# Performance work log

Measured on AMD Instinct MI355X. Metric: run time of the kernel, lower is better.

## Reference

```python
import jax, jax.numpy as jnp
import numpy as np

SPATIAL_SHAPES = [(128, 128), (64, 64), (32, 32), (16, 16)]  # (H_l, W_l) per level
NUM_HEADS = 8
NUM_LEVELS = 4
NUM_POINTS = 4
EMBED_DIM = 256
HEAD_DIM = EMBED_DIM // NUM_HEADS
LEN_V = sum(h * w for h, w in SPATIAL_SHAPES)  # 21760
BS, LQ = 8, 900


def setup_inputs() -> dict:
    key = jax.random.key(0)
    ks = jax.random.split(key, 12)
    s = 0.05
    return {
        'query': jax.random.normal(ks[0], (BS, LQ, EMBED_DIM), jnp.float32),
        'reference_points': jax.random.uniform(ks[1], (BS, LQ, NUM_LEVELS, 2), jnp.float32),
        'value': jax.random.normal(ks[2], (BS, LEN_V, EMBED_DIM), jnp.float32),
        'w_value': jax.random.normal(ks[3], (EMBED_DIM, EMBED_DIM), jnp.float32) * s,
        'b_value': jnp.zeros((EMBED_DIM,), jnp.float32),
        'w_off': jax.random.normal(ks[4], (EMBED_DIM, NUM_HEADS * NUM_LEVELS * NUM_POINTS * 2), jnp.float32) * s,
        'b_off': jax.random.normal(ks[5], (NUM_HEADS * NUM_LEVELS * NUM_POINTS * 2,), jnp.float32),
        'w_attn': jax.random.normal(ks[6], (EMBED_DIM, NUM_HEADS * NUM_LEVELS * NUM_POINTS), jnp.float32) * s,
        'b_attn': jnp.zeros((NUM_HEADS * NUM_LEVELS * NUM_POINTS,), jnp.float32),
        'w_out': jax.random.normal(ks[7], (EMBED_DIM, EMBED_DIM), jnp.float32) * s,
        'b_out': jnp.zeros((EMBED_DIM,), jnp.float32),
    }


def _bilinear_sample(val, locx, locy, H, W):
    # val: [bs, nh, H*W, hd]; locx/locy: [bs, nh, N] normalized in [0,1]
    # grid_sample semantics: align_corners=False, zero padding.
    px = locx * W - 0.5
    py = locy * H - 0.5
    x0 = jnp.floor(px)
    y0 = jnp.floor(py)
    dx = px - x0
    dy = py - y0
    x0i = x0.astype(jnp.int32)
    y0i = y0.astype(jnp.int32)
    out = jnp.zeros(val.shape[:2] + (locx.shape[-1], val.shape[-1]), val.dtype)
    corners = [
        (x0i, y0i, (1 - dx) * (1 - dy)),
        (x0i + 1, y0i, dx * (1 - dy)),
        (x0i, y0i + 1, (1 - dx) * dy),
        (x0i + 1, y0i + 1, dx * dy),
    ]
    for xi, yi, w in corners:
        valid = ((xi >= 0) & (xi < W) & (yi >= 0) & (yi < H)).astype(val.dtype)
        idx = jnp.clip(yi, 0, H - 1) * W + jnp.clip(xi, 0, W - 1)
        g = jnp.take_along_axis(val, idx[..., None], axis=2)  # [bs,nh,N,hd]
        out = out + g * (w * valid)[..., None]
    return out


def reference(query, reference_points, value, w_value, b_value, w_off, b_off,
              w_attn, b_attn, w_out, b_out):
    bs, Lq, C = query.shape
    # value projection -> [bs, Lv, nh, hd]
    v = (value @ w_value + b_value).reshape(bs, -1, NUM_HEADS, HEAD_DIM)
    # sampling offsets [bs,Lq,nh,L,P,2], attention weights softmax over L*P
    off = (query @ w_off + b_off).reshape(bs, Lq, NUM_HEADS, NUM_LEVELS, NUM_POINTS, 2)
    aw = (query @ w_attn + b_attn).reshape(bs, Lq, NUM_HEADS, NUM_LEVELS * NUM_POINTS)
    aw = jax.nn.softmax(aw, axis=-1).reshape(bs, Lq, NUM_HEADS, NUM_LEVELS, NUM_POINTS)
    # normalizer is (W_l, H_l) per level (flip of spatial shapes)
    norm = jnp.asarray([[w, h] for h, w in SPATIAL_SHAPES], query.dtype)  # [L,2]
    loc = reference_points[:, :, None, :, None, :] + off / norm[None, None, None, :, None, :]
    # per-level bilinear sampling and weighted reduction
    out = jnp.zeros((bs, Lq, NUM_HEADS, HEAD_DIM), query.dtype)
    start = 0
    for l, (H, W) in enumerate(SPATIAL_SHAPES):
        vl = v[:, start:start + H * W]                       # [bs,HW,nh,hd]
        vl = vl.transpose(0, 2, 1, 3)                        # [bs,nh,HW,hd]
        ll = loc[:, :, :, l].transpose(0, 2, 1, 3, 4)        # [bs,nh,Lq,P,2]
        ll = ll.reshape(bs, NUM_HEADS, Lq * NUM_POINTS, 2)
        s = _bilinear_sample(vl, ll[..., 0], ll[..., 1], H, W)
        s = s.reshape(bs, NUM_HEADS, Lq, NUM_POINTS, HEAD_DIM)
        out = out + jnp.einsum('bhqpd,bqhp->bqhd', s, aw[:, :, :, l])
        start += H * W
    out = out.reshape(bs, Lq, C)
    return out @ w_out + b_out
```

## Files before the change

kernel.cpp:

```cpp
#include <hip/hip_runtime.h>

#define BS 8
#define LQ 900
#define NH 8
#define NL 4
#define NP 4
#define HD 32
#define ED 256
#define LEN_V 21760

typedef __attribute__((ext_vector_type(8))) short bf16x8;
typedef __attribute__((ext_vector_type(4))) float f32x4;
typedef __attribute__((ext_vector_type(4))) float fv4;

static __device__ __forceinline__ unsigned short f2bf(float f) {
  union { float f; unsigned u; } x; x.f = f;
  unsigned r = x.u + 0x7fffu + ((x.u >> 16) & 1u);
  return (unsigned short)(r >> 16);
}
static __device__ __forceinline__ float bf2f(unsigned short s) {
  union { unsigned u; float f; } x; x.u = ((unsigned)s) << 16;
  return x.f;
}
static __device__ __forceinline__ unsigned pack2(float a, float b) {
  return (unsigned)f2bf(a) | ((unsigned)f2bf(b) << 16);
}
static __device__ __forceinline__ bf16x8 pack8(fv4 a, fv4 b) {
  union { uint4 u; bf16x8 h; } x;
  x.u.x = pack2(a.x, a.y);
  x.u.y = pack2(a.z, a.w);
  x.u.z = pack2(b.x, b.y);
  x.u.w = pack2(b.z, b.w);
  return x.h;
}

__global__ __launch_bounds__(256) void bprep_kernel(
    const float* __restrict__ w, unsigned short* __restrict__ Bsw) {
  const int id = blockIdx.x * 256 + threadIdx.x;
  const int n = id & 255;
  const int kseg = (id >> 8) & 3;
  const int kc = id >> 10;
  const float* src = &w[(kc * 32 + kseg * 8) * 256 + n];
  float f[8];
#pragma unroll
  for (int j = 0; j < 8; j++) f[j] = src[j * 256];
  uint4 pk;
  pk.x = pack2(f[0], f[1]);
  pk.y = pack2(f[2], f[3]);
  pk.z = pack2(f[4], f[5]);
  pk.w = pack2(f[6], f[7]);
  *(uint4*)&Bsw[((kc * 4 + kseg) * 256 + n) * 8] = pk;
}

__global__ __launch_bounds__(256, 3) void vproj_kernel(
    const float* __restrict__ value, const unsigned short* __restrict__ Bsw,
    const float* __restrict__ bias, unsigned short* __restrict__ vout) {
  const int t = threadIdx.x;
  const int row0 = blockIdx.x * 64;
  const int wv = t >> 6;
  const int lane = t & 63;
  const int quad = lane >> 4;
  const int nn = lane & 15;

  f32x4 acc[4][4];
#pragma unroll
  for (int i = 0; i < 4; i++)
#pragma unroll
    for (int j = 0; j < 4; j++) acc[i][j] = (f32x4)(0.f);

  const float* aptr = &value[(row0 + nn) * 256 + quad * 8];
  const unsigned short* bptr = &Bsw[(quad * 256 + wv * 64 + nn) * 8];

#pragma unroll
  for (int kc = 0; kc < 8; kc++) {
    bf16x8 af[4], bfr[4];
#pragma unroll
    for (int rt = 0; rt < 4; rt++) {
      const float* pa = aptr + rt * 16 * 256 + kc * 32;
      fv4 v0 = *(const fv4*)pa;
      fv4 v1 = *(const fv4*)(pa + 4);
      af[rt] = pack8(v0, v1);
    }
#pragma unroll
    for (int ct = 0; ct < 4; ct++)
      bfr[ct] = *(const bf16x8*)(bptr + (kc * 1024 + ct * 16) * 8);
#pragma unroll
    for (int rt = 0; rt < 4; rt++)
#pragma unroll
      for (int ct = 0; ct < 4; ct++)
        acc[rt][ct] = __builtin_amdgcn_mfma_f32_16x16x32_bf16(
            af[rt], bfr[ct], acc[rt][ct], 0, 0, 0);
  }

#pragma unroll
  for (int ct = 0; ct < 4; ct++) {
    const int col = wv * 64 + ct * 16 + nn;
    const float bv = bias[col];
    const int h = col >> 5;
    const int d = col & 31;
#pragma unroll
    for (int rt = 0; rt < 4; rt++) {
      f32x4 f = acc[rt][ct];
#pragma unroll
      for (int reg = 0; reg < 4; reg++) {
        const int grow = row0 + rt * 16 + quad * 4 + reg;
        const int b = grow / LEN_V;
        const int s = grow - b * LEN_V;
        vout[((b * NH + h) * LEN_V + s) * HD + d] = f2bf(f[reg] + bv);
      }
    }
  }
}

__global__ __launch_bounds__(384, 2) void offattn_kernel(
    const float* __restrict__ query,
    const float* __restrict__ w_off, const float* __restrict__ b_off,
    const float* __restrict__ w_attn, const float* __restrict__ b_attn,
    float* __restrict__ OFF, float* __restrict__ LOG) {
  const int t = threadIdx.x;
  const int row0 = blockIdx.x * 32;
  const int rg = t / 96;
  const int c4 = t % 96;
  const int col = c4 * 4;
  const bool isOff = col < 256;
  const float* wbase = isOff ? (w_off + col) : (w_attn + (col - 256));
  const int wstride = isOff ? 256 : 128;
  const float* bb = isOff ? (b_off + col) : (b_attn + (col - 256));
  __shared__ float a_lds[32][8];

  float4 acc[8];
#pragma unroll
  for (int r = 0; r < 8; r++) acc[r] = make_float4(0.f, 0.f, 0.f, 0.f);

  for (int k0 = 0; k0 < 256; k0 += 8) {
    __syncthreads();
    if (t < 256) a_lds[t >> 3][t & 7] = query[(row0 + (t >> 3)) * 256 + k0 + (t & 7)];
    __syncthreads();
    float4 wr[8];
#pragma unroll
    for (int k = 0; k < 8; k++)
      wr[k] = *(const float4*)&wbase[(k0 + k) * wstride];
#pragma unroll
    for (int r = 0; r < 8; r++) {
      const float* ar = &a_lds[rg * 8 + r][0];
      float4 a0 = *(const float4*)&ar[0];
      float4 a1 = *(const float4*)&ar[4];
      float4 s = acc[r];
      s.x += a0.x*wr[0].x + a0.y*wr[1].x + a0.z*wr[2].x + a0.w*wr[3].x
           + a1.x*wr[4].x + a1.y*wr[5].x + a1.z*wr[6].x + a1.w*wr[7].x;
      s.y += a0.x*wr[0].y + a0.y*wr[1].y + a0.z*wr[2].y + a0.w*wr[3].y
           + a1.x*wr[4].y + a1.y*wr[5].y + a1.z*wr[6].y + a1.w*wr[7].y;
      s.z += a0.x*wr[0].z + a0.y*wr[1].z + a0.z*wr[2].z + a0.w*wr[3].z
           + a1.x*wr[4].z + a1.y*wr[5].z + a1.z*wr[6].z + a1.w*wr[7].z;
      s.w += a0.x*wr[0].w + a0.y*wr[1].w + a0.z*wr[2].w + a0.w*wr[3].w
           + a1.x*wr[4].w + a1.y*wr[5].w + a1.z*wr[6].w + a1.w*wr[7].w;
      acc[r] = s;
    }
  }

  const float4 bv = *(const float4*)bb;
#pragma unroll
  for (int r = 0; r < 8; r++) {
    const int grow = row0 + rg * 8 + r;
    float4 o = make_float4(acc[r].x + bv.x, acc[r].y + bv.y,
                           acc[r].z + bv.z, acc[r].w + bv.w);
    if (isOff) *(float4*)&OFF[grow * 256 + col] = o;
    else       *(float4*)&LOG[grow * 128 + (col - 256)] = o;
  }
}

__global__ __launch_bounds__(256, 4) void sample_kernel(
    const float* __restrict__ refp, const unsigned short* __restrict__ vp,
    const float* __restrict__ OFF, const float* __restrict__ LOG,
    float* __restrict__ RES) {
  const int t = threadIdx.x;
  const int b = blockIdx.x / (LQ / 4);
  const int q0 = (blockIdx.x % (LQ / 4)) * 4;

  __shared__ float off_lds[4][256];
  __shared__ float aw_lds[4][128];
  __shared__ float ref_lds[4][4][2];
  __shared__ int   soff[512][4];
  __shared__ float swt[512][4];

#pragma unroll
  for (int qi = 0; qi < 4; qi++)
    off_lds[qi][t] = OFF[(b * LQ + q0 + qi) * 256 + t];
  if (t < 128) {
#pragma unroll
    for (int qi = 0; qi < 4; qi++)
      aw_lds[qi][t] = LOG[(b * LQ + q0 + qi) * 128 + t];
  }
  if (t < 32) {
    const int qi = t >> 3, l = (t >> 1) & 3, xy = t & 1;
    ref_lds[qi][l][xy] = refp[((b * LQ + q0 + qi) * NL + l) * 2 + xy];
  }
  __syncthreads();

  if (t < 32) {
    const int qi = t >> 3, h = t & 7;
    float* a = &aw_lds[qi][h * 16];
    float m = a[0];
#pragma unroll
    for (int i = 1; i < 16; i++) m = fmaxf(m, a[i]);
    float e[16];
    float ssum = 0.f;
#pragma unroll
    for (int i = 0; i < 16; i++) { e[i] = __expf(a[i] - m); ssum += e[i]; }
    const float inv = 1.f / ssum;
#pragma unroll
    for (int i = 0; i < 16; i++) a[i] = e[i] * inv;
  }
  __syncthreads();

#pragma unroll
  for (int ss = 0; ss < 2; ss++) {
    const int sid = t + ss * 256;
    const int p = sid & 3, l = (sid >> 2) & 3, h = (sid >> 4) & 7, qi = sid >> 7;
    const int W = 128 >> l;
    const int base = (l == 0) ? 0 : ((l == 1) ? 16384 : ((l == 2) ? 20480 : 21504));
    const float Wf = (float)W;
    const float refx = ref_lds[qi][l][0];
    const float refy = ref_lds[qi][l][1];
    const float offx = off_lds[qi][h * 32 + l * 8 + p * 2 + 0];
    const float offy = off_lds[qi][h * 32 + l * 8 + p * 2 + 1];
    const float aw = aw_lds[qi][h * 16 + l * 4 + p];
    const float px = refx * Wf + offx - 0.5f;
    const float py = refy * Wf + offy - 0.5f;
    const float x0f = floorf(px), y0f = floorf(py);
    const float dx = px - x0f, dy = py - y0f;
    const int x0 = (int)x0f, y0 = (int)y0f;
    const int x1 = x0 + 1, y1 = y0 + 1;
    const float mx0 = (x0 >= 0 && x0 < W) ? 1.f : 0.f;
    const float mx1 = (x1 >= 0 && x1 < W) ? 1.f : 0.f;
    const float my0 = (y0 >= 0 && y0 < W) ? 1.f : 0.f;
    const float my1 = (y1 >= 0 && y1 < W) ? 1.f : 0.f;
    const int x0c = min(max(x0, 0), W - 1);
    const int x1c = min(max(x1, 0), W - 1);
    const int y0c = min(max(y0, 0), W - 1);
    const int y1c = min(max(y1, 0), W - 1);
    soff[sid][0] = (base + y0c * W + x0c) * 16;
    soff[sid][1] = (base + y0c * W + x1c) * 16;
    soff[sid][2] = (base + y1c * W + x0c) * 16;
    soff[sid][3] = (base + y1c * W + x1c) * 16;
    swt[sid][0] = (1.f - dx) * (1.f - dy) * mx0 * my0 * aw;
    swt[sid][1] = dx * (1.f - dy) * mx1 * my0 * aw;
    swt[sid][2] = (1.f - dx) * dy * mx0 * my1 * aw;
    swt[sid][3] = dx * dy * mx1 * my1 * aw;
  }
  __syncthreads();

  const int qsel = t >> 7;
  const int hh = (t >> 4) & 7;
  const int d2 = t & 15;
  const unsigned* vpu = (const unsigned*)vp + (size_t)(b * NH + hh) * (LEN_V * HD / 2);
#pragma unroll
  for (int j = 0; j < 2; j++) {
    const int qi = qsel * 2 + j;
    float r0 = 0.f, r1 = 0.f;
#pragma unroll
    for (int lp = 0; lp < 16; lp++) {
      const int sid = ((qi * 8 + hh) << 4) + lp;
      const int4 o = *(const int4*)&soff[sid][0];
      const float4 w = *(const float4*)&swt[sid][0];
      const unsigned u00 = vpu[o.x + d2];
      const unsigned u10 = vpu[o.y + d2];
      const unsigned u01 = vpu[o.z + d2];
      const unsigned u11 = vpu[o.w + d2];
      r0 += w.x * bf2f((unsigned short)(u00 & 0xffff))
          + w.y * bf2f((unsigned short)(u10 & 0xffff))
          + w.z * bf2f((unsigned short)(u01 & 0xffff))
          + w.w * bf2f((unsigned short)(u11 & 0xffff));
      r1 += w.x * bf2f((unsigned short)(u00 >> 16))
          + w.y * bf2f((unsigned short)(u10 >> 16))
          + w.z * bf2f((unsigned short)(u01 >> 16))
          + w.w * bf2f((unsigned short)(u11 >> 16));
    }
    float2 rr = make_float2(r0, r1);
    *(float2*)&RES[(b * LQ + q0 + qi) * 256 + hh * 32 + d2 * 2] = rr;
  }
}

__global__ __launch_bounds__(256, 2) void outproj_kernel(
    const float* __restrict__ RES, const float* __restrict__ w,
    const float* __restrict__ bias, float* __restrict__ out) {
  const int t = threadIdx.x;
  const int row0 = blockIdx.x * 32;
  const int rg = t >> 6;
  const int c0 = (t & 63) << 2;
  __shared__ float a_lds[32][8];

  float4 acc[8];
#pragma unroll
  for (int r = 0; r < 8; r++) acc[r] = make_float4(0.f, 0.f, 0.f, 0.f);

  const int lr = t >> 3;
  const int lk = t & 7;
  for (int k0 = 0; k0 < 256; k0 += 8) {
    __syncthreads();
    a_lds[lr][lk] = RES[(row0 + lr) * 256 + k0 + lk];
    __syncthreads();
    float4 wr[8];
#pragma unroll
    for (int k = 0; k < 8; k++)
      wr[k] = *(const float4*)&w[(k0 + k) * 256 + c0];
#pragma unroll
    for (int r = 0; r < 8; r++) {
      const float* ar = &a_lds[rg * 8 + r][0];
      float4 a0 = *(const float4*)&ar[0];
      float4 a1 = *(const float4*)&ar[4];
      float4 s = acc[r];
      s.x += a0.x*wr[0].x + a0.y*wr[1].x + a0.z*wr[2].x + a0.w*wr[3].x
           + a1.x*wr[4].x + a1.y*wr[5].x + a1.z*wr[6].x + a1.w*wr[7].x;
      s.y += a0.x*wr[0].y + a0.y*wr[1].y + a0.z*wr[2].y + a0.w*wr[3].y
           + a1.x*wr[4].y + a1.y*wr[5].y + a1.z*wr[6].y + a1.w*wr[7].y;
      s.z += a0.x*wr[0].z + a0.y*wr[1].z + a0.z*wr[2].z + a0.w*wr[3].z
           + a1.x*wr[4].z + a1.y*wr[5].z + a1.z*wr[6].z + a1.w*wr[7].z;
      s.w += a0.x*wr[0].w + a0.y*wr[1].w + a0.z*wr[2].w + a0.w*wr[3].w
           + a1.x*wr[4].w + a1.y*wr[5].w + a1.z*wr[6].w + a1.w*wr[7].w;
      acc[r] = s;
    }
  }

  const float4 bv = *(const float4*)&bias[c0];
#pragma unroll
  for (int r = 0; r < 8; r++) {
    const int grow = row0 + rg * 8 + r;
    float4 o = make_float4(acc[r].x + bv.x, acc[r].y + bv.y,
                           acc[r].z + bv.z, acc[r].w + bv.w);
    *(float4*)&out[grow * 256 + c0] = o;
  }
}

extern "C" void kernel_launch(void* const* d_in, const int* in_sizes, int n_in,
                              void* d_out, int out_size, void* d_ws, size_t ws_size,
                              hipStream_t stream) {
  (void)in_sizes; (void)n_in; (void)out_size; (void)ws_size;
  const float* query   = (const float*)d_in[0];
  const float* refp    = (const float*)d_in[1];
  const float* value   = (const float*)d_in[2];
  const float* w_value = (const float*)d_in[3];
  const float* b_value = (const float*)d_in[4];
  const float* w_off   = (const float*)d_in[5];
  const float* b_off   = (const float*)d_in[6];
  const float* w_attn  = (const float*)d_in[7];
  const float* b_attn  = (const float*)d_in[8];
  const float* w_out   = (const float*)d_in[9];
  const float* b_out   = (const float*)d_in[10];
  float* out = (float*)d_out;

  char* ws = (char*)d_ws;
  unsigned short* vp = (unsigned short*)ws;
  float* OFF = (float*)(ws + 89128960);
  float* LOG = (float*)(ws + 89128960 + 7372800);
  float* RES = (float*)(ws + 89128960 + 7372800 + 3686400);
  unsigned short* Bsw = (unsigned short*)(ws + 89128960 + 7372800 + 3686400 + 7372800);

  bprep_kernel<<<32, 256, 0, stream>>>(w_value, Bsw);
  vproj_kernel<<<(BS * LEN_V) / 64, 256, 0, stream>>>(value, Bsw, b_value, vp);
  offattn_kernel<<<(BS * LQ) / 32, 384, 0, stream>>>(query, w_off, b_off,
                                                     w_attn, b_attn, OFF, LOG);
  sample_kernel<<<BS * (LQ / 4), 256, 0, stream>>>(refp, vp, OFF, LOG, RES);
  outproj_kernel<<<(BS * LQ) / 32, 256, 0, stream>>>(RES, w_out, b_out, out);
}
```

Measured before the change: 483.2 us.

## Stage value tile through LDS in vproj and widen sampling gathers to 8 bytes

In the value projection, each thread now loads one 8-float segment of the A tile with nontemporal loads, converts it to bf16 into shared memory, and the waves read their MFMA fragments from LDS. Before, every wave re-read the fp32 value rows from global memory. The epilogue's per-element batch division is hoisted out, and occupancy hints rise for both kernels. The sampling kernel now gives each thread 4 channels with 8-byte gathers instead of 2 channels with 4-byte gathers, which halves the gather instruction count but adds two barriers per k-chunk in vproj.

```diff
diff --git a/kernel.cpp b/kernel.cpp
--- a/kernel.cpp
+++ b/kernel.cpp
@@ -18,20 +18,16 @@
   unsigned r = x.u + 0x7fffu + ((x.u >> 16) & 1u);
   return (unsigned short)(r >> 16);
 }
-static __device__ __forceinline__ float bf2f(unsigned short s) {
-  union { unsigned u; float f; } x; x.u = ((unsigned)s) << 16;
+static __device__ __forceinline__ float bf_lo(unsigned u) {
+  union { unsigned u; float f; } x; x.u = u << 16;
+  return x.f;
+}
+static __device__ __forceinline__ float bf_hi(unsigned u) {
+  union { unsigned u; float f; } x; x.u = u & 0xffff0000u;
   return x.f;
 }
 static __device__ __forceinline__ unsigned pack2(float a, float b) {
   return (unsigned)f2bf(a) | ((unsigned)f2bf(b) << 16);
-}
-static __device__ __forceinline__ bf16x8 pack8(fv4 a, fv4 b) {
-  union { uint4 u; bf16x8 h; } x;
-  x.u.x = pack2(a.x, a.y);
-  x.u.y = pack2(a.z, a.w);
-  x.u.z = pack2(b.x, b.y);
-  x.u.w = pack2(b.z, b.w);
-  return x.h;
 }
 
 __global__ __launch_bounds__(256) void bprep_kernel(
@@ -52,7 +48,7 @@
   *(uint4*)&Bsw[((kc * 4 + kseg) * 256 + n) * 8] = pk;
 }
 
-__global__ __launch_bounds__(256, 3) void vproj_kernel(
+__global__ __launch_bounds__(256, 4) void vproj_kernel(
     const float* __restrict__ value, const unsigned short* __restrict__ Bsw,
     const float* __restrict__ bias, unsigned short* __restrict__ vout) {
   const int t = threadIdx.x;
@@ -62,28 +58,40 @@
   const int quad = lane >> 4;
   const int nn = lane & 15;
 
+  __shared__ unsigned short a_lds[4 * 64 * 8];
+
   f32x4 acc[4][4];
 #pragma unroll
   for (int i = 0; i < 4; i++)
 #pragma unroll
     for (int j = 0; j < 4; j++) acc[i][j] = (f32x4)(0.f);
 
-  const float* aptr = &value[(row0 + nn) * 256 + quad * 8];
+  const int arow = t >> 2;
+  const int akseg = t & 3;
   const unsigned short* bptr = &Bsw[(quad * 256 + wv * 64 + nn) * 8];
 
-#pragma unroll
   for (int kc = 0; kc < 8; kc++) {
+    __syncthreads();
+    {
+      const float* pa = &value[(row0 + arow) * 256 + kc * 32 + akseg * 8];
+      fv4 v0 = __builtin_nontemporal_load((const fv4*)pa);
+      fv4 v1 = __builtin_nontemporal_load((const fv4*)(pa + 4));
+      uint4 pk;
+      pk.x = pack2(v0.x, v0.y);
+      pk.y = pack2(v0.z, v0.w);
+      pk.z = pack2(v1.x, v1.y);
+      pk.w = pack2(v1.z, v1.w);
+      *(uint4*)&a_lds[(akseg * 64 + arow) * 8] = pk;
+    }
+    __syncthreads();
+
     bf16x8 af[4], bfr[4];
-#pragma unroll
-    for (int rt = 0; rt < 4; rt++) {
-      const float* pa = aptr + rt * 16 * 256 + kc * 32;
-      fv4 v0 = *(const fv4*)pa;
-      fv4 v1 = *(const fv4*)(pa + 4);
-      af[rt] = pack8(v0, v1);
-    }
 #pragma unroll
     for (int ct = 0; ct < 4; ct++)
       bfr[ct] = *(const bf16x8*)(bptr + (kc * 1024 + ct * 16) * 8);
+#pragma unroll
+    for (int rt = 0; rt < 4; rt++)
+      af[rt] = *(const bf16x8*)&a_lds[(quad * 64 + rt * 16 + nn) * 8];
 #pragma unroll
     for (int rt = 0; rt < 4; rt++)
 #pragma unroll
@@ -92,21 +100,22 @@
             af[rt], bfr[ct], acc[rt][ct], 0, 0, 0);
   }
 
+  const int bb = row0 / LEN_V;
+  const int s0 = row0 - bb * LEN_V;
 #pragma unroll
   for (int ct = 0; ct < 4; ct++) {
     const int col = wv * 64 + ct * 16 + nn;
     const float bv = bias[col];
     const int h = col >> 5;
     const int d = col & 31;
+    unsigned short* vb = &vout[((bb * NH + h) * LEN_V + s0) * HD + d];
 #pragma unroll
     for (int rt = 0; rt < 4; rt++) {
       f32x4 f = acc[rt][ct];
 #pragma unroll
       for (int reg = 0; reg < 4; reg++) {
-        const int grow = row0 + rt * 16 + quad * 4 + reg;
-        const int b = grow / LEN_V;
-        const int s = grow - b * LEN_V;
-        vout[((b * NH + h) * LEN_V + s) * HD + d] = f2bf(f[reg] + bv);
+        const int s = rt * 16 + quad * 4 + reg;
+        vb[s * HD] = f2bf(f[reg] + bv);
       }
     }
   }
@@ -169,7 +178,7 @@
   }
 }
 
-__global__ __launch_bounds__(256, 4) void sample_kernel(
+__global__ __launch_bounds__(256, 6) void sample_kernel(
     const float* __restrict__ refp, const unsigned short* __restrict__ vp,
     const float* __restrict__ OFF, const float* __restrict__ LOG,
     float* __restrict__ RES) {
@@ -239,10 +248,10 @@
     const int x1c = min(max(x1, 0), W - 1);
     const int y0c = min(max(y0, 0), W - 1);
     const int y1c = min(max(y1, 0), W - 1);
-    soff[sid][0] = (base + y0c * W + x0c) * 16;
-    soff[sid][1] = (base + y0c * W + x1c) * 16;
-    soff[sid][2] = (base + y1c * W + x0c) * 16;
-    soff[sid][3] = (base + y1c * W + x1c) * 16;
+    soff[sid][0] = (base + y0c * W + x0c) * 8;
+    soff[sid][1] = (base + y0c * W + x1c) * 8;
+    soff[sid][2] = (base + y1c * W + x0c) * 8;
+    soff[sid][3] = (base + y1c * W + x1c) * 8;
     swt[sid][0] = (1.f - dx) * (1.f - dy) * mx0 * my0 * aw;
     swt[sid][1] = dx * (1.f - dy) * mx1 * my0 * aw;
     swt[sid][2] = (1.f - dx) * dy * mx0 * my1 * aw;
@@ -250,35 +259,28 @@
   }
   __syncthreads();
 
-  const int qsel = t >> 7;
-  const int hh = (t >> 4) & 7;
-  const int d2 = t & 15;
-  const unsigned* vpu = (const unsigned*)vp + (size_t)(b * NH + hh) * (LEN_V * HD / 2);
-#pragma unroll
-  for (int j = 0; j < 2; j++) {
-    const int qi = qsel * 2 + j;
-    float r0 = 0.f, r1 = 0.f;
-#pragma unroll
-    for (int lp = 0; lp < 16; lp++) {
-      const int sid = ((qi * 8 + hh) << 4) + lp;
-      const int4 o = *(const int4*)&soff[sid][0];
-      const float4 w = *(const float4*)&swt[sid][0];
-      const unsigned u00 = vpu[o.x + d2];
-      const unsigned u10 = vpu[o.y + d2];
-      const unsigned u01 = vpu[o.z + d2];
-      const unsigned u11 = vpu[o.w + d2];
-      r0 += w.x * bf2f((unsigned short)(u00 & 0xffff))
-          + w.y * bf2f((unsigned short)(u10 & 0xffff))
-          + w.z * bf2f((unsigned short)(u01 & 0xffff))
-          + w.w * bf2f((unsigned short)(u11 & 0xffff));
-      r1 += w.x * bf2f((unsigned short)(u00 >> 16))
-          + w.y * bf2f((unsigned short)(u10 >> 16))
-          + w.z * bf2f((unsigned short)(u01 >> 16))
-          + w.w * bf2f((unsigned short)(u11 >> 16));
-    }
-    float2 rr = make_float2(r0, r1);
-    *(float2*)&RES[(b * LQ + q0 + qi) * 256 + hh * 32 + d2 * 2] = rr;
-  }
+  const int qi = t >> 6;
+  const int hh = (t >> 3) & 7;
+  const int d4 = t & 7;
+  const uint2* vpu2 = (const uint2*)vp + (size_t)(b * NH + hh) * (LEN_V * HD / 4);
+  float r0 = 0.f, r1 = 0.f, r2 = 0.f, r3 = 0.f;
+  const int sbase = (qi * 8 + hh) << 4;
+#pragma unroll 4
+  for (int lp = 0; lp < 16; lp++) {
+    const int sid = sbase + lp;
+    const int4 o = *(const int4*)&soff[sid][0];
+    const float4 w = *(const float4*)&swt[sid][0];
+    const uint2 u00 = vpu2[o.x + d4];
+    const uint2 u10 = vpu2[o.y + d4];
+    const uint2 u01 = vpu2[o.z + d4];
+    const uint2 u11 = vpu2[o.w + d4];
+    r0 += w.x * bf_lo(u00.x) + w.y * bf_lo(u10.x) + w.z * bf_lo(u01.x) + w.w * bf_lo(u11.x);
+    r1 += w.x * bf_hi(u00.x) + w.y * bf_hi(u10.x) + w.z * bf_hi(u01.x) + w.w * bf_hi(u11.x);
+    r2 += w.x * bf_lo(u00.y) + w.y * bf_lo(u10.y) + w.z * bf_lo(u01.y) + w.w * bf_lo(u11.y);
+    r3 += w.x * bf_hi(u00.y) + w.y * bf_hi(u10.y) + w.z * bf_hi(u01.y) + w.w * bf_hi(u11.y);
+  }
+  float4 rr = make_float4(r0, r1, r2, r3);
+  *(float4*)&RES[(b * LQ + q0 + qi) * 256 + hh * 32 + d4 * 4] = rr;
 }
 
 __global__ __launch_bounds__(256, 2) void outproj_kernel(
```

After: 422.6 us. 1.14x faster.
